# Performance work log

Measured on AMD Instinct MI355X. Metric: run time of the kernel, lower is better.

Reference implementation:

```python
import jax, jax.numpy as jnp
import numpy as np

N = 50000          # nodes
E = 800000         # edges
D_IN, D_HID, D_OUT = 256, 128, 64
NUM_GRAPHS = 16
BN_EPS = 1e-5


def gcn_conv(x, src, dst, W, b, n_nodes):
    """PyG GCNConv: add self-loops, sym-normalized aggregation, then bias."""
    loop = jnp.arange(n_nodes, dtype=src.dtype)
    s = jnp.concatenate([src, loop])
    d = jnp.concatenate([dst, loop])
    deg = jax.ops.segment_sum(jnp.ones_like(s, dtype=x.dtype), d, num_segments=n_nodes)
    dinv = jax.lax.rsqrt(jnp.maximum(deg, 1.0))  # deg >= 1 due to self-loops
    norm = dinv[s] * dinv[d]                      # [E+N]
    h = x @ W                                     # [N, out]
    msg = h[s] * norm[:, None]                    # gather + scale
    out = jax.ops.segment_sum(msg, d, num_segments=n_nodes)
    return out + b


def batch_norm(x, gamma, beta):
    mu = jnp.mean(x, axis=0)
    var = jnp.mean(jnp.square(x - mu), axis=0)
    return (x - mu) * jax.lax.rsqrt(var + BN_EPS) * gamma + beta


def setup_inputs() -> dict:
    key = jax.random.key(0)
    ks = jax.random.split(key, 10)
    x = jax.random.normal(ks[0], (N, D_IN), dtype=jnp.float32)
    edge_index = jax.random.randint(ks[1], (2, E), 0, N, dtype=jnp.int64)
    batch = jnp.sort(jax.random.randint(ks[2], (N,), 0, NUM_GRAPHS, dtype=jnp.int64))
    def glorot(k, fan_in, fan_out):
        lim = np.sqrt(6.0 / (fan_in + fan_out))
        return jax.random.uniform(k, (fan_in, fan_out), jnp.float32, -lim, lim)
    return {
        "x": x, "edge_index": edge_index, "batch": batch,
        "W1": glorot(ks[3], D_IN, D_HID),  "b1": jnp.zeros((D_HID,), jnp.float32),
        "W2": glorot(ks[4], D_HID, D_HID), "b2": jnp.zeros((D_HID,), jnp.float32),
        "W3": glorot(ks[5], D_HID, D_OUT), "b3": jnp.zeros((D_OUT,), jnp.float32),
        "g1": jnp.ones((D_HID,), jnp.float32), "be1": jnp.zeros((D_HID,), jnp.float32),
        "g2": jnp.ones((D_HID,), jnp.float32), "be2": jnp.zeros((D_HID,), jnp.float32),
    }


def reference(x, edge_index, batch, W1, b1, W2, b2, W3, b3, g1, be1, g2, be2):
    src, dst = edge_index[0], edge_index[1]
    n = x.shape[0]
    h = gcn_conv(x, src, dst, W1, b1, n)
    h = jax.nn.relu(batch_norm(h, g1, be1))
    h = gcn_conv(h, src, dst, W2, b2, n)
    h = jax.nn.relu(batch_norm(h, g2, be2))
    h = gcn_conv(h, src, dst, W3, b3, n)          # [N, D_OUT]
    # global mean pool over graph ids
    sums = jax.ops.segment_sum(h, batch, num_segments=NUM_GRAPHS)
    cnts = jax.ops.segment_sum(jnp.ones((n,), h.dtype), batch, num_segments=NUM_GRAPHS)
    return sums / jnp.maximum(cnts, 1.0)[:, None]  # [NUM_GRAPHS, D_OUT]
```

## Files before the change

kernel.cpp:

```cpp
#include <hip/hip_runtime.h>
#include <hip/hip_bf16.h>

#define D_IN   256
#define D_HID  128
#define D_OUT_ 64
#define NGRAPH 16
#define BN_EPS 1e-5f

#define SCAN_TPB 256
#define SCAN_VPT 4

typedef __attribute__((ext_vector_type(8))) short short8;
typedef __attribute__((ext_vector_type(4))) float floatx4;

__device__ __forceinline__ unsigned short f2bf(float x) {
    unsigned u = __float_as_uint(x);
    return (unsigned short)((u + 0x7fffu + ((u >> 16) & 1u)) >> 16);
}
__device__ __forceinline__ unsigned pack2bf(float lo, float hi) {
    return (unsigned)f2bf(lo) | ((unsigned)f2bf(hi) << 16);
}
__device__ __forceinline__ void bf2_decode(unsigned u, float& lo, float& hi) {
    lo = __uint_as_float(u << 16);
    hi = __uint_as_float(u & 0xffff0000u);
}
__device__ __forceinline__ void accum8(float* acc, uint4 qv, float wt) {
    float f0,f1,f2,f3,f4,f5,f6,f7;
    bf2_decode(qv.x, f0, f1); bf2_decode(qv.y, f2, f3);
    bf2_decode(qv.z, f4, f5); bf2_decode(qv.w, f6, f7);
    acc[0]=fmaf(f0,wt,acc[0]); acc[1]=fmaf(f1,wt,acc[1]);
    acc[2]=fmaf(f2,wt,acc[2]); acc[3]=fmaf(f3,wt,acc[3]);
    acc[4]=fmaf(f4,wt,acc[4]); acc[5]=fmaf(f5,wt,acc[5]);
    acc[6]=fmaf(f6,wt,acc[6]); acc[7]=fmaf(f7,wt,acc[7]);
}

__global__ void count_rank_kernel(const int* __restrict__ dst, int E,
                                  int* __restrict__ deg, int* __restrict__ rank) {
    int e0 = blockIdx.x * (256 * 4) + threadIdx.x;
    int d[4];
    #pragma unroll
    for (int i = 0; i < 4; ++i) {
        int e = e0 + i * 256;
        if (e < E) d[i] = dst[e];
    }
    #pragma unroll
    for (int i = 0; i < 4; ++i) {
        int e = e0 + i * 256;
        if (e < E) rank[e] = atomicAdd(&deg[d[i]], 1);
    }
}

__global__ void dinv_bsum_kernel(const int* __restrict__ deg, int N,
                                 float* __restrict__ dinv, int* __restrict__ bsum) {
    __shared__ int red[SCAN_TPB];
    int t = threadIdx.x;
    int base = blockIdx.x * (SCAN_TPB * SCAN_VPT) + t;
    int s = 0;
    #pragma unroll
    for (int i = 0; i < SCAN_VPT; ++i) {
        int idx = base + i * SCAN_TPB;
        if (idx < N) {
            int d = deg[idx];
            dinv[idx] = rsqrtf((float)(d + 1));
            s += d;
        }
    }
    red[t] = s;
    __syncthreads();
    for (int off = SCAN_TPB / 2; off > 0; off >>= 1) {
        if (t < off) red[t] += red[t + off];
        __syncthreads();
    }
    if (t == 0) bsum[blockIdx.x] = red[0];
}

__global__ void scan_bsum_kernel(const int* __restrict__ bsum, int NB,
                                 int* __restrict__ bprefix,
                                 int* __restrict__ rowstart, int N, int E) {
    __shared__ int part[SCAN_TPB];
    int t = threadIdx.x;
    int s = (t < NB) ? bsum[t] : 0;
    part[t] = s;
    __syncthreads();
    for (int off = 1; off < SCAN_TPB; off <<= 1) {
        int x = (t >= off) ? part[t - off] : 0;
        __syncthreads();
        part[t] += x;
        __syncthreads();
    }
    if (t < NB) bprefix[t] = part[t] - s;
    if (t == 0) rowstart[N] = E;
}

__global__ void local_scan_kernel(const int* __restrict__ deg, int N,
                                  const int* __restrict__ bprefix,
                                  int* __restrict__ rowstart) {
    __shared__ int part[SCAN_TPB];
    int t = threadIdx.x;
    int base = blockIdx.x * (SCAN_TPB * SCAN_VPT) + t * SCAN_VPT;
    int v[SCAN_VPT];
    int s = 0;
    #pragma unroll
    for (int i = 0; i < SCAN_VPT; ++i) {
        v[i] = (base + i < N) ? deg[base + i] : 0;
        s += v[i];
    }
    part[t] = s;
    __syncthreads();
    for (int off = 1; off < SCAN_TPB; off <<= 1) {
        int x = (t >= off) ? part[t - off] : 0;
        __syncthreads();
        part[t] += x;
        __syncthreads();
    }
    int excl = part[t] - s + bprefix[blockIdx.x];
    #pragma unroll
    for (int i = 0; i < SCAN_VPT; ++i) {
        if (base + i < N) rowstart[base + i] = excl;
        excl += v[i];
    }
}

__global__ void scatter_kernel(const int* __restrict__ src, const int* __restrict__ dst,
                               int E, const int* __restrict__ rowstart,
                               const int* __restrict__ rank, int* __restrict__ csr) {
    int e0 = blockIdx.x * (256 * 4) + threadIdx.x;
    int d[4], rk[4], sv[4], pos[4];
    #pragma unroll
    for (int i = 0; i < 4; ++i) {
        int e = e0 + i * 256;
        if (e < E) { d[i] = dst[e]; rk[i] = rank[e]; sv[i] = src[e]; }
    }
    #pragma unroll
    for (int i = 0; i < 4; ++i) {
        int e = e0 + i * 256;
        if (e < E) pos[i] = rowstart[d[i]];
    }
    #pragma unroll
    for (int i = 0; i < 4; ++i) {
        int e = e0 + i * 256;
        if (e < E) csr[pos[i] + rk[i]] = sv[i];
    }
}

__global__ void wprep_all_kernel(const float* __restrict__ W1, const float* __restrict__ W2,
                                 const float* __restrict__ W3,
                                 unsigned short* __restrict__ Wt1,
                                 unsigned short* __restrict__ Wt2,
                                 unsigned short* __restrict__ Wt3) {
    int idx = blockIdx.x * blockDim.x + threadIdx.x;
    const int S1 = D_IN * D_HID;
    const int S2 = D_HID * D_HID;
    const int S3 = D_HID * D_OUT_;
    if (idx < S1) {
        int k = idx / D_HID, n = idx - k * D_HID;
        Wt1[(size_t)n * D_IN + k] = f2bf(W1[idx]);
    } else if (idx < S1 + S2) {
        int i = idx - S1;
        int k = i / D_HID, n = i - k * D_HID;
        Wt2[(size_t)n * D_HID + k] = f2bf(W2[i]);
    } else if (idx < S1 + S2 + S3) {
        int i = idx - S1 - S2;
        int k = i / D_OUT_, n = i - k * D_OUT_;
        Wt3[(size_t)n * D_HID + k] = f2bf(W3[i]);
    }
}

template<int K, int NOUT, int FUSE, int ABF16>
__device__ __forceinline__ void gemm_body(
        int bid, const void* __restrict__ Aptr, const unsigned short* __restrict__ Wt,
        unsigned short* __restrict__ Cb, int M,
        const float* __restrict__ sums, const float* __restrict__ sumsq,
        const float* __restrict__ gam, const float* __restrict__ bet, float invN) {
    constexpr int NT = NOUT / 16;
    constexpr int KS = K / 32;
    __shared__ float s_sc[FUSE ? K : 1];
    __shared__ float s_sh[FUSE ? K : 1];
    if (FUSE) {
        int t = threadIdx.x;
        if (t < K) {
            float mu  = sums[t] * invN;
            float var = sumsq[t] * invN - mu * mu;
            float sc  = gam[t] * rsqrtf(var + BN_EPS);
            s_sc[t] = sc;
            s_sh[t] = fmaf(-mu, sc, bet[t]);
        }
        __syncthreads();
    }
    int lane = threadIdx.x & 63;
    int wave = threadIdx.x >> 6;
    int col  = lane & 15;
    int quad = lane >> 4;
    int kq   = quad * 8;
    int row  = bid * 64 + wave * 16 + col;
    int rowc = min(row, M - 1);

    short8 afr[KS];
    if (ABF16) {
        const unsigned short* Ab = (const unsigned short*)Aptr;
        uint4 q[KS];
        #pragma unroll
        for (int i = 0; i < KS; ++i)
            q[i] = *(const uint4*)&Ab[(size_t)rowc * K + i * 32 + kq];
        __builtin_amdgcn_sched_barrier(0);
        #pragma unroll
        for (int i = 0; i < KS; ++i) {
            if (FUSE) {
                int kb = i * 32 + kq;
                float f0,f1,f2,f3,f4,f5,f6,f7;
                bf2_decode(q[i].x, f0, f1); bf2_decode(q[i].y, f2, f3);
                bf2_decode(q[i].z, f4, f5); bf2_decode(q[i].w, f6, f7);
                float4 sc0 = *(const float4*)&s_sc[kb];
                float4 sc1 = *(const float4*)&s_sc[kb + 4];
                float4 sh0 = *(const float4*)&s_sh[kb];
                float4 sh1 = *(const float4*)&s_sh[kb + 4];
                f0 = fmaxf(0.f, fmaf(f0, sc0.x, sh0.x));
                f1 = fmaxf(0.f, fmaf(f1, sc0.y, sh0.y));
                f2 = fmaxf(0.f, fmaf(f2, sc0.z, sh0.z));
                f3 = fmaxf(0.f, fmaf(f3, sc0.w, sh0.w));
                f4 = fmaxf(0.f, fmaf(f4, sc1.x, sh1.x));
                f5 = fmaxf(0.f, fmaf(f5, sc1.y, sh1.y));
                f6 = fmaxf(0.f, fmaf(f6, sc1.z, sh1.z));
                f7 = fmaxf(0.f, fmaf(f7, sc1.w, sh1.w));
                uint4 p;
                p.x = pack2bf(f0, f1); p.y = pack2bf(f2, f3);
                p.z = pack2bf(f4, f5); p.w = pack2bf(f6, f7);
                afr[i] = __builtin_bit_cast(short8, p);
            } else {
                afr[i] = __builtin_bit_cast(short8, q[i]);
            }
        }
    } else {
        const float* Af = (const float*)Aptr;
        float4 a0[KS], a1[KS];
        #pragma unroll
        for (int i = 0; i < KS; ++i) {
            a0[i] = *(const float4*)&Af[(size_t)rowc * K + i * 32 + kq];
            a1[i] = *(const float4*)&Af[(size_t)rowc * K + i * 32 + kq + 4];
        }
        __builtin_amdgcn_sched_barrier(0);
        #pragma unroll
        for (int i = 0; i < KS; ++i) {
            uint4 p;
            p.x = pack2bf(a0[i].x, a0[i].y); p.y = pack2bf(a0[i].z, a0[i].w);
            p.z = pack2bf(a1[i].x, a1[i].y); p.w = pack2bf(a1[i].z, a1[i].w);
            afr[i] = __builtin_bit_cast(short8, p);
        }
    }

    floatx4 acc[NT];
    #pragma unroll
    for (int nt = 0; nt < NT; ++nt) acc[nt] = (floatx4){0.f, 0.f, 0.f, 0.f};

    #pragma unroll
    for (int i = 0; i < KS; ++i) {
        #pragma unroll
        for (int nt = 0; nt < NT; ++nt) {
            short8 bfrag = *(const short8*)&Wt[(size_t)(nt * 16 + col) * K + i * 32 + kq];
            acc[nt] = __builtin_amdgcn_mfma_f32_16x16x32_bf16(afr[i], bfrag, acc[nt], 0, 0, 0);
        }
    }

    int obase = bid * 64 + wave * 16 + quad * 4;
    #pragma unroll
    for (int r = 0; r < 4; ++r) {
        int orow = obase + r;
        if (orow < M) {
            #pragma unroll
            for (int nt = 0; nt < NT; ++nt)
                Cb[(size_t)orow * NOUT + nt * 16 + col] = f2bf(acc[nt][r]);
        }
    }
}

template<int K, int NOUT, int FUSE, int ABF16>
__global__ __launch_bounds__(256, 3) void gemm_mfma_kernel(
        const void* __restrict__ Aptr, const unsigned short* __restrict__ Wt,
        unsigned short* __restrict__ Cb, int M,
        const float* __restrict__ sums, const float* __restrict__ sumsq,
        const float* __restrict__ gam, const float* __restrict__ bet, float invN) {
    gemm_body<K, NOUT, FUSE, ABF16>(blockIdx.x, Aptr, Wt, Cb, M, sums, sumsq, gam, bet, invN);
}

template<int D>
__global__ __launch_bounds__(256) void agg_bf16_kernel(
        const unsigned short* __restrict__ h, const float* __restrict__ dinv,
        const int* __restrict__ rowstart, const int* __restrict__ csr,
        const float* __restrict__ bias,
        unsigned short* __restrict__ outb, int N) {
    constexpr int LPR = D / 8;
    constexpr int RPB = 256 / LPR;
    int lane = threadIdx.x & (LPR - 1);
    int r    = threadIdx.x / LPR;
    int v = blockIdx.x * RPB + r;
    if (v >= N) return;
    int c0 = lane * 8;
    const unsigned short* hc = h + c0;
    float dv = dinv[v];

    float acc[8];
    {
        float w = dv * dv;
        uint4 q = *(const uint4*)&hc[(size_t)v * D];
        float4 b0 = *(const float4*)&bias[c0];
        float4 b1 = *(const float4*)&bias[c0 + 4];
        acc[0]=b0.x; acc[1]=b0.y; acc[2]=b0.z; acc[3]=b0.w;
        acc[4]=b1.x; acc[5]=b1.y; acc[6]=b1.z; acc[7]=b1.w;
        accum8(acc, q, w);
    }

    int j  = rowstart[v];
    int j1 = rowstart[v + 1];
    for (; j + 8 <= j1; j += 8) {
        int   s[8]; float w[8]; uint4 q[8];
        #pragma unroll
        for (int i = 0; i < 8; ++i) s[i] = csr[j + i];
        #pragma unroll
        for (int i = 0; i < 8; ++i) q[i] = *(const uint4*)&hc[(size_t)s[i] * D];
        #pragma unroll
        for (int i = 0; i < 8; ++i) w[i] = dinv[s[i]] * dv;
        #pragma unroll
        for (int i = 0; i < 8; ++i) accum8(acc, q[i], w[i]);
    }
    for (; j + 4 <= j1; j += 4) {
        int s0 = csr[j],     s1 = csr[j + 1];
        int s2 = csr[j + 2], s3 = csr[j + 3];
        float w0 = dinv[s0] * dv, w1 = dinv[s1] * dv;
        float w2 = dinv[s2] * dv, w3 = dinv[s3] * dv;
        uint4 q0 = *(const uint4*)&hc[(size_t)s0 * D];
        uint4 q1 = *(const uint4*)&hc[(size_t)s1 * D];
        uint4 q2 = *(const uint4*)&hc[(size_t)s2 * D];
        uint4 q3 = *(const uint4*)&hc[(size_t)s3 * D];
        accum8(acc, q0, w0); accum8(acc, q1, w1);
        accum8(acc, q2, w2); accum8(acc, q3, w3);
    }
    for (; j < j1; ++j) {
        int s = csr[j];
        float w = dinv[s] * dv;
        uint4 q = *(const uint4*)&hc[(size_t)s * D];
        accum8(acc, q, w);
    }

    uint4 o;
    o.x = pack2bf(acc[0], acc[1]); o.y = pack2bf(acc[2], acc[3]);
    o.z = pack2bf(acc[4], acc[5]); o.w = pack2bf(acc[6], acc[7]);
    *(uint4*)&outb[(size_t)v * D + c0] = o;
}

__global__ void bn_stats_bf16_kernel(const unsigned short* __restrict__ x, int N,
                                     float* __restrict__ sums, float* __restrict__ sumsq) {
    __shared__ float ls0[256], ls1[256], lq0[256], lq1[256];
    int pr = threadIdx.x & 63;
    int rg = threadIdx.x >> 6;
    float s0=0.f, s1=0.f, q0=0.f, q1=0.f;
    for (int v = blockIdx.x * 4 + rg; v < N; v += gridDim.x * 4) {
        unsigned u = *(const unsigned*)&x[(size_t)v * 128 + pr * 2];
        float lo, hi; bf2_decode(u, lo, hi);
        s0 += lo; s1 += hi;
        q0 = fmaf(lo, lo, q0); q1 = fmaf(hi, hi, q1);
    }
    ls0[threadIdx.x]=s0; ls1[threadIdx.x]=s1; lq0[threadIdx.x]=q0; lq1[threadIdx.x]=q1;
    __syncthreads();
    if (threadIdx.x < 64) {
        int pp = threadIdx.x;
        float a0=0,a1=0,b0=0,b1=0;
        #pragma unroll
        for (int g = 0; g < 4; ++g) {
            a0 += ls0[g*64+pp]; a1 += ls1[g*64+pp];
            b0 += lq0[g*64+pp]; b1 += lq1[g*64+pp];
        }
        atomicAdd(&sums[pp*2],  a0); atomicAdd(&sums[pp*2+1],  a1);
        atomicAdd(&sumsq[pp*2], b0); atomicAdd(&sumsq[pp*2+1], b1);
    }
}

__global__ void pool_bf16_kernel(const unsigned short* __restrict__ x,
                                 const int* __restrict__ batch, int N,
                                 float* __restrict__ psum, int* __restrict__ pcnt) {
    __shared__ float ls[NGRAPH * 64];
    __shared__ int   lc[NGRAPH];
    for (int i = threadIdx.x; i < NGRAPH * 64; i += blockDim.x) ls[i] = 0.f;
    if (threadIdx.x < NGRAPH) lc[threadIdx.x] = 0;
    __syncthreads();
    int total = N * 32;
    for (int idx = blockIdx.x * blockDim.x + threadIdx.x; idx < total;
         idx += gridDim.x * blockDim.x) {
        int v = idx >> 5, cp = idx & 31;
        unsigned u = *(const unsigned*)&x[(size_t)v * 64 + cp * 2];
        float lo, hi; bf2_decode(u, lo, hi);
        int g = batch[v];
        atomicAdd(&ls[g * 64 + cp * 2],     lo);
        atomicAdd(&ls[g * 64 + cp * 2 + 1], hi);
        if (cp == 0) atomicAdd(&lc[g], 1);
    }
    __syncthreads();
    for (int i = threadIdx.x; i < NGRAPH * 64; i += blockDim.x) atomicAdd(&psum[i], ls[i]);
    if (threadIdx.x < NGRAPH) atomicAdd(&pcnt[threadIdx.x], lc[threadIdx.x]);
}

__global__ void pool_final_kernel(const float* __restrict__ psum, const int* __restrict__ pcnt,
                                  float* __restrict__ out) {
    int i = threadIdx.x;
    int g = i >> 6;
    float cnt = (float)max(pcnt[g], 1);
    out[i] = psum[i] / cnt;
}

extern "C" void kernel_launch(void* const* d_in, const int* in_sizes, int n_in,
                              void* d_out, int out_size, void* d_ws, size_t ws_size,
                              hipStream_t stream) {
    const float* x   = (const float*)d_in[0];
    const int*   ei  = (const int*)d_in[1];
    const int*   bat = (const int*)d_in[2];
    const float* W1  = (const float*)d_in[3];
    const float* b1  = (const float*)d_in[4];
    const float* W2  = (const float*)d_in[5];
    const float* b2  = (const float*)d_in[6];
    const float* W3  = (const float*)d_in[7];
    const float* b3  = (const float*)d_in[8];
    const float* g1  = (const float*)d_in[9];
    const float* be1 = (const float*)d_in[10];
    const float* g2  = (const float*)d_in[11];
    const float* be2 = (const float*)d_in[12];
    float* out = (float*)d_out;

    int N = in_sizes[0] / D_IN;
    int E = in_sizes[1] / 2;
    const int* src = ei;
    const int* dst = ei + E;

    char* p = (char*)d_ws;
    auto alloc = [&](size_t bytes) { char* r = p; p += (bytes + 255) & ~(size_t)255; return r; };
    int NB = (N + SCAN_TPB * SCAN_VPT - 1) / (SCAN_TPB * SCAN_VPT);
    char*  zbase    = p;
    int*   deg      = (int*)  alloc((size_t)N * 4);
    float* sums1    = (float*)alloc(128 * 4);
    float* sumsq1   = (float*)alloc(128 * 4);
    float* sums2    = (float*)alloc(128 * 4);
    float* sumsq2   = (float*)alloc(128 * 4);
    float* psum     = (float*)alloc(NGRAPH * 64 * 4);
    int*   pcnt     = (int*)  alloc(NGRAPH * 4);
    size_t zspan    = (size_t)(p - zbase);
    int*   rowstart = (int*)  alloc((size_t)(N + 1) * 4);
    int*   rank     = (int*)  alloc((size_t)E * 4);
    float* dinv     = (float*)alloc((size_t)N * 4);
    int*   bsum     = (int*)  alloc((size_t)NB * 4);
    int*   bprefix  = (int*)  alloc((size_t)NB * 4);
    int*   csr      = (int*)  alloc((size_t)E * 4);
    unsigned short* hb16   = (unsigned short*)alloc((size_t)N * 128 * 2);
    unsigned short* aggb16 = (unsigned short*)alloc((size_t)N * 128 * 2);
    unsigned short* Wt1 = (unsigned short*)alloc((size_t)D_HID * D_IN * 2);
    unsigned short* Wt2 = (unsigned short*)alloc((size_t)D_HID * D_HID * 2);
    unsigned short* Wt3 = (unsigned short*)alloc((size_t)D_OUT_ * D_HID * 2);

    int ebl4 = (E + 1023) / 1024;
    int gblocks = (N + 63) / 64;
    float invN = 1.0f / (float)N;
    int wtot = D_IN * D_HID + D_HID * D_HID + D_HID * D_OUT_;

    (void)hipMemsetAsync(zbase, 0, zspan, stream);
    wprep_all_kernel<<<(wtot + 255) / 256, 256, 0, stream>>>(W1, W2, W3, Wt1, Wt2, Wt3);

    count_rank_kernel<<<ebl4, 256, 0, stream>>>(dst, E, deg, rank);
    dinv_bsum_kernel<<<NB, SCAN_TPB, 0, stream>>>(deg, N, dinv, bsum);
    scan_bsum_kernel<<<1, SCAN_TPB, 0, stream>>>(bsum, NB, bprefix, rowstart, N, E);
    local_scan_kernel<<<NB, SCAN_TPB, 0, stream>>>(deg, N, bprefix, rowstart);
    scatter_kernel<<<ebl4, 256, 0, stream>>>(src, dst, E, rowstart, rank, csr);

    gemm_mfma_kernel<D_IN, D_HID, 0, 0><<<gblocks, 256, 0, stream>>>(
        x, Wt1, hb16, N, nullptr, nullptr, nullptr, nullptr, 0.f);

    agg_bf16_kernel<D_HID><<<(N + 15) / 16, 256, 0, stream>>>(
        hb16, dinv, rowstart, csr, b1, aggb16, N);
    bn_stats_bf16_kernel<<<256, 256, 0, stream>>>(aggb16, N, sums1, sumsq1);

    gemm_mfma_kernel<D_HID, D_HID, 1, 1><<<gblocks, 256, 0, stream>>>(
        aggb16, Wt2, hb16, N, sums1, sumsq1, g1, be1, invN);
    agg_bf16_kernel<D_HID><<<(N + 15) / 16, 256, 0, stream>>>(
        hb16, dinv, rowstart, csr, b2, aggb16, N);
    bn_stats_bf16_kernel<<<256, 256, 0, stream>>>(aggb16, N, sums2, sumsq2);

    gemm_mfma_kernel<D_HID, D_OUT_, 1, 1><<<gblocks, 256, 0, stream>>>(
        aggb16, Wt3, hb16, N, sums2, sumsq2, g2, be2, invN);
    agg_bf16_kernel<D_OUT_><<<(N + 31) / 32, 256, 0, stream>>>(
        hb16, dinv, rowstart, csr, b3, aggb16, N);

    pool_bf16_kernel<<<256, 256, 0, stream>>>(aggb16, bat, N, psum, pcnt);
    pool_final_kernel<<<1, NGRAPH * 64, 0, stream>>>(psum, pcnt, out);
}
```

Before: 400.7 us.

## Stage transposed weights in swizzled LDS for MFMA GEMM B-fragments

Each GEMM block now copies the whole bf16 weight matrix into shared memory, using an XOR swizzle to avoid bank conflicts, and reads MFMA B fragments from LDS instead of global memory. The A-row loads are issued before the weight copy so the two overlap. Launch bounds drop from 3 to 2 blocks per SU to allow for the larger LDS use (up to 64KB for the 256x128 layer). This trades repeated global/L2 weight reads for a per-block LDS fill and lower occupancy.

```diff
diff --git a/kernel.cpp b/kernel.cpp
--- a/kernel.cpp
+++ b/kernel.cpp
@@ -174,8 +174,47 @@
         const float* __restrict__ gam, const float* __restrict__ bet, float invN) {
     constexpr int NT = NOUT / 16;
     constexpr int KS = K / 32;
+    constexpr int CHUNKS = NOUT * K / 8;
+    constexpr int KROW16 = K / 8;
+    __shared__ unsigned short s_wt[NOUT * K];
     __shared__ float s_sc[FUSE ? K : 1];
     __shared__ float s_sh[FUSE ? K : 1];
+
+    int lane = threadIdx.x & 63;
+    int wave = threadIdx.x >> 6;
+    int col  = lane & 15;
+    int quad = lane >> 4;
+    int kq   = quad * 8;
+    int row  = bid * 64 + wave * 16 + col;
+    int rowc = min(row, M - 1);
+
+    uint4  qa[ABF16 ? KS : 1];
+    float4 a0[ABF16 ? 1 : KS], a1[ABF16 ? 1 : KS];
+    if (ABF16) {
+        const unsigned short* Ab = (const unsigned short*)Aptr;
+        #pragma unroll
+        for (int i = 0; i < KS; ++i)
+            qa[i] = *(const uint4*)&Ab[(size_t)rowc * K + i * 32 + kq];
+    } else {
+        const float* Af = (const float*)Aptr;
+        #pragma unroll
+        for (int i = 0; i < KS; ++i) {
+            a0[i] = *(const float4*)&Af[(size_t)rowc * K + i * 32 + kq];
+            a1[i] = *(const float4*)&Af[(size_t)rowc * K + i * 32 + kq + 4];
+        }
+    }
+
+    {
+        const uint4* Wg = (const uint4*)Wt;
+        #pragma unroll
+        for (int it = 0; it < CHUNKS / 256; ++it) {
+            int c = it * 256 + (int)threadIdx.x;
+            uint4 v = Wg[c];
+            int n = c / KROW16;
+            unsigned byte = ((unsigned)c * 16u) ^ ((unsigned)(n & 7) << 4);
+            *(uint4*)((char*)s_wt + byte) = v;
+        }
+    }
     if (FUSE) {
         int t = threadIdx.x;
         if (t < K) {
@@ -185,31 +224,18 @@
             s_sc[t] = sc;
             s_sh[t] = fmaf(-mu, sc, bet[t]);
         }
-        __syncthreads();
-    }
-    int lane = threadIdx.x & 63;
-    int wave = threadIdx.x >> 6;
-    int col  = lane & 15;
-    int quad = lane >> 4;
-    int kq   = quad * 8;
-    int row  = bid * 64 + wave * 16 + col;
-    int rowc = min(row, M - 1);
+    }
+    __syncthreads();
 
     short8 afr[KS];
     if (ABF16) {
-        const unsigned short* Ab = (const unsigned short*)Aptr;
-        uint4 q[KS];
-        #pragma unroll
-        for (int i = 0; i < KS; ++i)
-            q[i] = *(const uint4*)&Ab[(size_t)rowc * K + i * 32 + kq];
-        __builtin_amdgcn_sched_barrier(0);
         #pragma unroll
         for (int i = 0; i < KS; ++i) {
             if (FUSE) {
                 int kb = i * 32 + kq;
                 float f0,f1,f2,f3,f4,f5,f6,f7;
-                bf2_decode(q[i].x, f0, f1); bf2_decode(q[i].y, f2, f3);
-                bf2_decode(q[i].z, f4, f5); bf2_decode(q[i].w, f6, f7);
+                bf2_decode(qa[i].x, f0, f1); bf2_decode(qa[i].y, f2, f3);
+                bf2_decode(qa[i].z, f4, f5); bf2_decode(qa[i].w, f6, f7);
                 float4 sc0 = *(const float4*)&s_sc[kb];
                 float4 sc1 = *(const float4*)&s_sc[kb + 4];
                 float4 sh0 = *(const float4*)&s_sh[kb];
@@ -227,18 +253,10 @@
                 p.z = pack2bf(f4, f5); p.w = pack2bf(f6, f7);
                 afr[i] = __builtin_bit_cast(short8, p);
             } else {
-                afr[i] = __builtin_bit_cast(short8, q[i]);
+                afr[i] = __builtin_bit_cast(short8, qa[i]);
             }
         }
     } else {
-        const float* Af = (const float*)Aptr;
-        float4 a0[KS], a1[KS];
-        #pragma unroll
-        for (int i = 0; i < KS; ++i) {
-            a0[i] = *(const float4*)&Af[(size_t)rowc * K + i * 32 + kq];
-            a1[i] = *(const float4*)&Af[(size_t)rowc * K + i * 32 + kq + 4];
-        }
-        __builtin_amdgcn_sched_barrier(0);
         #pragma unroll
         for (int i = 0; i < KS; ++i) {
             uint4 p;
@@ -256,7 +274,9 @@
     for (int i = 0; i < KS; ++i) {
         #pragma unroll
         for (int nt = 0; nt < NT; ++nt) {
-            short8 bfrag = *(const short8*)&Wt[(size_t)(nt * 16 + col) * K + i * 32 + kq];
+            unsigned byte = ((unsigned)((nt * 16 + col) * K + i * 32 + kq)) * 2u;
+            byte ^= (unsigned)(col & 7) << 4;
+            short8 bfrag = *(const short8*)((const char*)s_wt + byte);
             acc[nt] = __builtin_amdgcn_mfma_f32_16x16x32_bf16(afr[i], bfrag, acc[nt], 0, 0, 0);
         }
     }
@@ -274,7 +294,7 @@
 }
 
 template<int K, int NOUT, int FUSE, int ABF16>
-__global__ __launch_bounds__(256, 3) void gemm_mfma_kernel(
+__global__ __launch_bounds__(256, 2) void gemm_mfma_kernel(
         const void* __restrict__ Aptr, const unsigned short* __restrict__ Wt,
         unsigned short* __restrict__ Cb, int M,
         const float* __restrict__ sums, const float* __restrict__ sumsq,
```

Result: faster. 357.0 us (-10.9%).
